# Kernel optimization log

Measured on AMD Instinct MI355X. Metric: run time of the kernel, lower is better.

The kernel has to match this reference:

```python
import jax, jax.numpy as jnp
import numpy as np

D_MODEL = 2048
N_HEADS = 16
HEAD_DIM = D_MODEL // N_HEADS  # 128
B, S = 4, 2048


def setup_inputs() -> dict:
    key = jax.random.key(0)
    ks = jax.random.split(key, 7)
    scale = 1.0 / np.sqrt(D_MODEL)
    return {
        "x": jax.random.normal(ks[0], (B, S, D_MODEL), dtype=jnp.float32),
        "cos": jax.random.uniform(ks[1], (S, HEAD_DIM // 2), dtype=jnp.float32),
        "sin": jax.random.uniform(ks[2], (S, HEAD_DIM // 2), dtype=jnp.float32),
        "Wq": jax.random.normal(ks[3], (D_MODEL, D_MODEL), dtype=jnp.float32) * scale,
        "Wk": jax.random.normal(ks[4], (D_MODEL, D_MODEL), dtype=jnp.float32) * scale,
        "Wv": jax.random.normal(ks[5], (D_MODEL, D_MODEL), dtype=jnp.float32) * scale,
        "Wo": jax.random.normal(ks[6], (D_MODEL, D_MODEL), dtype=jnp.float32) * scale,
    }


def apply_rope(x, cos, sin):
    # x: [B, H, S, head_dim]; cos/sin: [S, half] (split-in-half RoPE)
    half = x.shape[-1] // 2
    x1, x2 = x[..., :half], x[..., half:]
    cos = cos[None, None, :, :].astype(x.dtype)
    sin = sin[None, None, :, :].astype(x.dtype)
    return jnp.concatenate([x1 * cos - x2 * sin, x1 * sin + x2 * cos], axis=-1)


def reference(x, cos, sin, Wq, Wk, Wv, Wo):
    Bx, Sx, _ = x.shape
    # nn.Linear: y = x @ W.T
    def proj(W):
        y = jnp.einsum("bsd,ed->bse", x, W)
        return y.reshape(Bx, Sx, N_HEADS, HEAD_DIM).transpose(0, 2, 1, 3)  # [B,H,S,hd]
    q = apply_rope(proj(Wq), cos, sin)
    k = apply_rope(proj(Wk), cos, sin)
    v = proj(Wv)
    scale = 1.0 / np.sqrt(HEAD_DIM)
    scores = jnp.einsum("bhqd,bhkd->bhqk", q, k) * scale  # [B,H,S,S]
    attn = jax.nn.softmax(scores, axis=-1)
    out = jnp.einsum("bhqk,bhkd->bhqd", attn, v)
    out = out.transpose(0, 2, 1, 3).reshape(Bx, Sx, D_MODEL)
    return jnp.einsum("bsd,ed->bse", out, Wo)
```

## Files before the change

### kernel.cpp

```cpp
#include <hip/hip_runtime.h>

typedef _Float16 half_t;
typedef __attribute__((ext_vector_type(8))) _Float16 half8;
typedef __attribute__((ext_vector_type(4))) _Float16 half4v;
typedef __attribute__((ext_vector_type(4))) float f32x4;

#define MFMA16(a,b,c) __builtin_amdgcn_mfma_f32_16x16x32_f16((a),(b),(c),0,0,0)

__device__ __forceinline__ void gld_lds16(const half_t* g, half_t* l){
    __builtin_amdgcn_global_load_lds((__attribute__((address_space(1))) void*)(g),
                                     (__attribute__((address_space(3))) void*)(l), 16, 0, 0);
}

__global__ __launch_bounds__(256) void cvt_k(const float* __restrict__ s, half_t* __restrict__ d, int n4){
    int i = blockIdx.x * 256 + threadIdx.x;
    if (i < n4){
        float4 v = ((const float4*)s)[i];
        half4v h = { (half_t)v.x, (half_t)v.y, (half_t)v.z, (half_t)v.w };
        ((half4v*)d)[i] = h;
    }
}

__global__ __launch_bounds__(256) void cvtw_k(const float* __restrict__ w0, const float* __restrict__ w1,
                                              const float* __restrict__ w2, const float* __restrict__ w3,
                                              half_t* __restrict__ dst){
    const float* srcs[4] = {w0, w1, w2, w3};
    const float* s = srcs[blockIdx.y];
    int i = blockIdx.x * 256 + threadIdx.x;
    float4 v = ((const float4*)s)[i];
    half4v h = { (half_t)v.x, (half_t)v.y, (half_t)v.z, (half_t)v.w };
    ((half4v*)(dst))[(size_t)blockIdx.y * 1048576 + i] = h;
}

#define VMWAIT_(n) asm volatile("s_waitcnt vmcnt(" #n ")" ::: "memory")
#define VMWAIT(n)  VMWAIT_(n)

#define STAGE8(hh) { \
    const int Tt2 = (hh) >> 2, jj2 = (hh) & 3; \
    half_t* db = smem + ((jj2 & 1) << 15) + ((Tt2 & 1) << 14) + ((jj2 >> 1) << 13); \
    const half_t* Gs = ((jj2 & 1) ? Bg : Ag) + Tt2*64 + ((jj2 >> 1) << 5); \
    gld_lds16(Gs + off0, db + d0); \
    gld_lds16(Gs + off1, db + d1); \
}

#define PHASE8(Tt, jj, hh, VMN) { \
    half_t* Ah = smem + (((Tt) & 1) << 14) + (((jj) >> 1) << 13); \
    half_t* Bh = Ah + 32768; \
    half8 af[4], bf[4]; \
    _Pragma("unroll") for (int x = 0; x < 4; x++) af[x] = *(const half8*)(Ah + (((jj)&1)*4 + x)*1024 + cA); \
    _Pragma("unroll") for (int y = 0; y < 4; y++) bf[y] = *(const half8*)(Bh + y*1024 + cB); \
    if ((hh) < 128) STAGE8(hh); \
    if ((jj) & 1) VMWAIT(VMN); \
    asm volatile("s_barrier" ::: "memory"); \
    __builtin_amdgcn_s_setprio(1); \
    _Pragma("unroll") for (int x = 0; x < 4; x++) \
      _Pragma("unroll") for (int y = 0; y < 4; y++) \
        acc[((jj)&1)*4 + x][y] = MFMA16(af[x], bf[y], acc[((jj)&1)*4 + x][y]); \
    __builtin_amdgcn_s_setprio(0); \
    __builtin_amdgcn_sched_barrier(0); \
    asm volatile("s_barrier" ::: "memory"); \
}

__global__ __launch_bounds__(512) void gemm8(const half_t* __restrict__ A, const half_t* __restrict__ B,
                                             half_t* __restrict__ Qw, half_t* __restrict__ Kw,
                                             half_t* __restrict__ Vt, float* __restrict__ Co, int kind){
    const int tid  = threadIdx.x;
    const int lane = tid & 63;
    const int w4   = lane >> 4;
    const int l15  = lane & 15;
    const int l7   = lane & 7;
    const int wav  = tid >> 6;
    const int wavM = wav >> 2;
    const int wnq  = wav & 3;

    const int nwg = gridDim.x;
    const int wg  = blockIdx.x;
    const int swz = (wg & 7) * (nwg >> 3) + (wg >> 3);
    const int bm  = swz & 31;
    const int bn  = swz >> 5;

    __shared__ __align__(16) half_t smem[65536];

    const half_t* Ag = A + (size_t)bm * 256 * 2048;
    const half_t* Bg = B + (size_t)bn * 256 * 2048;

    const int p0  = tid >> 3, q0 = tid & 7, c0 = q0 ^ (p0 & 7);
    const int off0 = (p0 + ((c0 >> 2) << 7)) * 2048 + ((c0 & 3) << 3);
    const int off1 = off0 + 131072;
    const int d0  = tid * 8, d1 = d0 + 4096;

    const int cA = l15*64 + (((w4 | (wavM << 2)) ^ l7) << 3);
    const int cB = ((wnq & 1)*64 + l15)*64 + (((w4 | ((wnq >> 1) << 2)) ^ l7) << 3);

    f32x4 acc[8][4] = {};

#pragma unroll
    for (int h = 0; h < 6; h++) STAGE8(h);
    VMWAIT(4);
    asm volatile("s_barrier" ::: "memory");

    for (int it = 0; it < 15; it++){
        const int h0 = it*8 + 6;
        PHASE8(2*it,   0, h0,     6); PHASE8(2*it,   1, h0 + 1, 6);
        PHASE8(2*it,   2, h0 + 2, 6); PHASE8(2*it,   3, h0 + 3, 6);
        PHASE8(2*it+1, 0, h0 + 4, 6); PHASE8(2*it+1, 1, h0 + 5, 6);
        PHASE8(2*it+1, 2, h0 + 6, 6); PHASE8(2*it+1, 3, h0 + 7, 6);
    }
    PHASE8(30, 0, 126, 6); PHASE8(30, 1, 127, 6);
    PHASE8(30, 2, 128, 6); PHASE8(30, 3, 129, 2);
    PHASE8(31, 0, 130, 0); PHASE8(31, 1, 131, 0);
    PHASE8(31, 2, 132, 0); PHASE8(31, 3, 133, 0);

    const int mB = bm*256 + wavM*128 + w4*4;
    const int nB = bn*256 + wnq*64 + l15;

    if (kind == 0){
#pragma unroll
        for (int mi = 0; mi < 8; mi++)
#pragma unroll
            for (int ni = 0; ni < 4; ni++){
                int n  = nB + ni*16;
                int which = n >> 11;
                int nb = n & 2047;
                int m0 = mB + mi*16;
                if (which < 2){
                    half_t* dst = which ? Kw : Qw;
#pragma unroll
                    for (int r = 0; r < 4; r++){
                        int m = m0 + r;
                        dst[(((size_t)(m >> 11)*16 + (nb >> 7))*2048 + (m & 2047))*128 + (nb & 127)] = (half_t)acc[mi][ni][r];
                    }
                } else {
                    half4v hv = {(half_t)acc[mi][ni][0], (half_t)acc[mi][ni][1],
                                 (half_t)acc[mi][ni][2], (half_t)acc[mi][ni][3]};
                    *(half4v*)(Vt + (((size_t)(m0 >> 11)*16 + (nb >> 7))*128 + (nb & 127))*2048 + (m0 & 2047)) = hv;
                }
            }
    } else {
#pragma unroll
        for (int mi = 0; mi < 8; mi++)
#pragma unroll
            for (int ni = 0; ni < 4; ni++){
                int n  = nB + ni*16;
                int m0 = mB + mi*16;
#pragma unroll
                for (int r = 0; r < 4; r++)
                    Co[(size_t)(m0 + r)*2048 + n] = acc[mi][ni][r];
            }
    }
}

__global__ __launch_bounds__(256) void rope_k(half_t* __restrict__ Qw, half_t* __restrict__ Kw,
                                              const float* __restrict__ cs, const float* __restrict__ sn){
    int t  = blockIdx.x * 256 + threadIdx.x;
    int d  = t & 63;
    int s  = (t >> 6) & 2047;
    int bh = t >> 17;
    float c  = cs[s*64 + d];
    float si = sn[s*64 + d];
    size_t base = ((size_t)bh*2048 + s)*128 + d;
    float q1 = (float)Qw[base], q2 = (float)Qw[base+64];
    Qw[base]    = (half_t)(q1*c - q2*si);
    Qw[base+64] = (half_t)(q1*si + q2*c);
    float k1 = (float)Kw[base], k2 = (float)Kw[base+64];
    Kw[base]    = (half_t)(k1*c - k2*si);
    Kw[base+64] = (half_t)(k1*si + k2*c);
}

__global__ __launch_bounds__(256, 3) void attn_k(const half_t* __restrict__ Q, const half_t* __restrict__ K,
                                                 const half_t* __restrict__ Vt, half_t* __restrict__ AO){
    const int tid  = threadIdx.x;
    const int lane = tid & 63;
    const int w    = lane >> 4;
    const int l15  = lane & 15;
    const int l7   = lane & 7;
    const int wav  = tid >> 6;
    const int qt   = blockIdx.x;
    const int bh   = blockIdx.y;

    __shared__ __align__(16) half_t smem[8192 + 8192 + 4*2304];
    half_t* Ks = smem;
    half_t* Vs = smem + 8192;
    half_t* Ps = smem + 16384 + wav*2304;
    half_t* Ob = smem + wav*4096;

    const half_t* Qb = Q + ((size_t)bh*2048 + qt*128 + wav*32)*128;
    half8 aq[2][4];
#pragma unroll
    for (int qi = 0; qi < 2; qi++)
#pragma unroll
        for (int ks = 0; ks < 4; ks++)
            aq[qi][ks] = *(const half8*)(Qb + (qi*16 + l15)*128 + ks*32 + w*8);

    f32x4 oacc[8][2] = {};
    float m_[2] = {-1e30f, -1e30f};
    float l_[2] = {0.0f, 0.0f};

    const float SSC = 0.08838834764831845f * 1.4426950408889634f;

    for (int kt = 0; kt < 32; kt++){
        const half_t* Kb = K  + ((size_t)bh*2048 + kt*64)*128;
        const half_t* Vb = Vt + (size_t)bh*128*2048 + kt*64;
        __syncthreads();
#pragma unroll
        for (int i = 0; i < 4; i++){
            int c = tid + i*256;
            int key = c >> 4, pc = c & 15;
            gld_lds16(Kb + key*128 + ((pc ^ (key&7)) << 3), Ks + c*8);
        }
#pragma unroll
        for (int i = 0; i < 4; i++){
            int c = tid + i*256;
            int d = c >> 3, pc = c & 7;
            gld_lds16(Vb + (size_t)d*2048 + ((pc ^ (d&7)) << 3), Vs + c*8);
        }
        __syncthreads();

        f32x4 sacc[4][2] = {};
#pragma unroll
        for (int ks = 0; ks < 4; ks++){
#pragma unroll
            for (int t = 0; t < 4; t++){
                half8 kf = *(const half8*)(Ks + (t*16 + l15)*128 + (((ks*4 + w) ^ l7) << 3));
                sacc[t][0] = MFMA16(kf, aq[0][ks], sacc[t][0]);
                sacc[t][1] = MFMA16(kf, aq[1][ks], sacc[t][1]);
            }
        }

#pragma unroll
        for (int qi = 0; qi < 2; qi++){
            float mx = sacc[0][qi][0];
#pragma unroll
            for (int t = 0; t < 4; t++)
#pragma unroll
                for (int r = 0; r < 4; r++) mx = fmaxf(mx, sacc[t][qi][r]);
            mx = fmaxf(mx, __shfl_xor(mx, 16));
            mx = fmaxf(mx, __shfl_xor(mx, 32));
            float mxs = mx * SSC;
            unsigned long long upd = __ballot(mxs > m_[qi]);
            if (upd){
                float mn    = fmaxf(m_[qi], mxs);
                float alpha = exp2f(m_[qi] - mn);
                m_[qi] = mn;
                l_[qi] *= alpha;
#pragma unroll
                for (int t = 0; t < 8; t++)
#pragma unroll
                    for (int r = 0; r < 4; r++) oacc[t][qi][r] *= alpha;
            }
            float mq = m_[qi];
            float sum = 0.0f;
#pragma unroll
            for (int t = 0; t < 4; t++){
                float p0 = exp2f(sacc[t][qi][0]*SSC - mq);
                float p1 = exp2f(sacc[t][qi][1]*SSC - mq);
                float p2 = exp2f(sacc[t][qi][2]*SSC - mq);
                float p3 = exp2f(sacc[t][qi][3]*SSC - mq);
                sum += (p0 + p1) + (p2 + p3);
                half4v hv = {(half_t)p0, (half_t)p1, (half_t)p2, (half_t)p3};
                *(half4v*)(Ps + (qi*16 + l15)*72 + t*16 + w*4) = hv;
            }
            sum += __shfl_xor(sum, 16);
            sum += __shfl_xor(sum, 32);
            l_[qi] += sum;
        }

#pragma unroll
        for (int c2 = 0; c2 < 2; c2++){
            half8 pf0 = *(const half8*)(Ps + l15*72        + c2*32 + w*8);
            half8 pf1 = *(const half8*)(Ps + (16 + l15)*72 + c2*32 + w*8);
#pragma unroll
            for (int t = 0; t < 8; t++){
                half8 vf = *(const half8*)(Vs + (t*16 + l15)*64 + (((c2*4 + w) ^ l7) << 3));
                oacc[t][0] = MFMA16(vf, pf0, oacc[t][0]);
                oacc[t][1] = MFMA16(vf, pf1, oacc[t][1]);
            }
        }
    }

    float inv[2] = {1.0f / l_[0], 1.0f / l_[1]};
    __syncthreads();
#pragma unroll
    for (int t = 0; t < 8; t++)
#pragma unroll
        for (int qi = 0; qi < 2; qi++){
            int q  = qi*16 + l15;
            int c8 = t*2 + (w>>1);
            int pc = c8 ^ l7;
            half4v hv = {(half_t)(oacc[t][qi][0]*inv[qi]), (half_t)(oacc[t][qi][1]*inv[qi]),
                         (half_t)(oacc[t][qi][2]*inv[qi]), (half_t)(oacc[t][qi][3]*inv[qi])};
            *(half4v*)(Ob + q*128 + pc*8 + (w&1)*4) = hv;
        }
    const int b = bh >> 4, h = bh & 15;
#pragma unroll
    for (int it = 0; it < 8; it++){
        int q  = it*4 + w;
        half8 rd = *(const half8*)(Ob + q*128 + ((l15 ^ (q&7)) << 3));
        int s = qt*128 + wav*32 + q;
        *(half8*)(AO + ((size_t)(b*2048 + s))*2048 + h*128 + l15*8) = rd;
    }
}

extern "C" void kernel_launch(void* const* d_in, const int* in_sizes, int n_in,
                              void* d_out, int out_size, void* d_ws, size_t ws_size,
                              hipStream_t stream){
    const float* x  = (const float*)d_in[0];
    const float* cs = (const float*)d_in[1];
    const float* sn = (const float*)d_in[2];
    const float* Wq = (const float*)d_in[3];
    const float* Wk = (const float*)d_in[4];
    const float* Wv = (const float*)d_in[5];
    const float* Wo = (const float*)d_in[6];

    half_t* ws = (half_t*)d_ws;
    half_t* xh = ws;
    half_t* w4 = ws + (size_t)16777216;
    half_t* qw = ws + (size_t)33554432;
    half_t* kw = ws + (size_t)50331648;
    half_t* vt = ws + (size_t)67108864;
    half_t* ao = ws + (size_t)83886080;

    cvt_k<<<16384, 256, 0, stream>>>(x, xh, 4194304);
    cvtw_k<<<dim3(4096, 4), 256, 0, stream>>>(Wq, Wk, Wv, Wo, w4);

    gemm8<<<768, 512, 0, stream>>>(xh, w4, qw, kw, vt, nullptr, 0);
    rope_k<<<32768, 256, 0, stream>>>(qw, kw, cs, sn);
    attn_k<<<dim3(16, 64), 256, 0, stream>>>(qw, kw, vt, ao);
    gemm8<<<256, 512, 0, stream>>>(ao, w4 + 12582912, nullptr, nullptr, nullptr,
                                   (float*)d_out, 1);
}
```

Before: 733.4 us.

## Register-prefetch next K/V tile in attention, fold scale into Q, remap blocks

The attention kernel now loads the next K/V tile into registers while computing the current one, then writes it to LDS after a barrier. This replaces the synchronous direct-to-LDS loads that stalled every iteration. The softmax scale is pre-multiplied into Q in fp16, which removes per-element multiplies but adds a small rounding risk. The grid is flattened and remapped so that consecutive blocks spread across heads, with the aim of improving cache locality. The register staging costs extra VGPRs and may reduce occupancy.

```diff
diff --git a/kernel.cpp b/kernel.cpp
--- a/kernel.cpp
+++ b/kernel.cpp
@@ -175,8 +175,9 @@
     const int l15  = lane & 15;
     const int l7   = lane & 7;
     const int wav  = tid >> 6;
-    const int qt   = blockIdx.x;
-    const int bh   = blockIdx.y;
+    const int bid  = blockIdx.x;
+    const int qt   = (bid >> 3) & 15;
+    const int bh   = (bid & 7) * 8 + (bid >> 7);
 
     __shared__ __align__(16) half_t smem[8192 + 8192 + 4*2304];
     half_t* Ks = smem;
@@ -184,37 +185,57 @@
     half_t* Ps = smem + 16384 + wav*2304;
     half_t* Ob = smem + wav*4096;
 
+    const float SSC = 0.08838834764831845f * 1.4426950408889634f;
+
     const half_t* Qb = Q + ((size_t)bh*2048 + qt*128 + wav*32)*128;
     half8 aq[2][4];
 #pragma unroll
     for (int qi = 0; qi < 2; qi++)
 #pragma unroll
-        for (int ks = 0; ks < 4; ks++)
-            aq[qi][ks] = *(const half8*)(Qb + (qi*16 + l15)*128 + ks*32 + w*8);
+        for (int ks = 0; ks < 4; ks++){
+            half8 t = *(const half8*)(Qb + (qi*16 + l15)*128 + ks*32 + w*8);
+            aq[qi][ks] = t * (half_t)SSC;
+        }
+
+    int koff[4], voff[4], soff[4];
+#pragma unroll
+    for (int i = 0; i < 4; i++){
+        int c = tid + i*256;
+        int key = c >> 4, pk = c & 15;
+        koff[i] = key*128 + ((pk ^ (key & 7)) << 3);
+        int d = c >> 3, pv = c & 7;
+        voff[i] = (d << 11) + ((pv ^ (d & 7)) << 3);
+        soff[i] = c * 8;
+    }
+
+    const half_t* Kbase = K  + (size_t)bh*2048*128;
+    const half_t* Vbase = Vt + (size_t)bh*128*2048;
+
+    float4 kst[4], vst[4];
+#pragma unroll
+    for (int i = 0; i < 4; i++) kst[i] = *(const float4*)(Kbase + koff[i]);
+#pragma unroll
+    for (int i = 0; i < 4; i++) vst[i] = *(const float4*)(Vbase + voff[i]);
+#pragma unroll
+    for (int i = 0; i < 4; i++) *(float4*)(Ks + soff[i]) = kst[i];
+#pragma unroll
+    for (int i = 0; i < 4; i++) *(float4*)(Vs + soff[i]) = vst[i];
+    __syncthreads();
 
     f32x4 oacc[8][2] = {};
     float m_[2] = {-1e30f, -1e30f};
     float l_[2] = {0.0f, 0.0f};
 
-    const float SSC = 0.08838834764831845f * 1.4426950408889634f;
-
     for (int kt = 0; kt < 32; kt++){
-        const half_t* Kb = K  + ((size_t)bh*2048 + kt*64)*128;
-        const half_t* Vb = Vt + (size_t)bh*128*2048 + kt*64;
-        __syncthreads();
-#pragma unroll
-        for (int i = 0; i < 4; i++){
-            int c = tid + i*256;
-            int key = c >> 4, pc = c & 15;
-            gld_lds16(Kb + key*128 + ((pc ^ (key&7)) << 3), Ks + c*8);
-        }
-#pragma unroll
-        for (int i = 0; i < 4; i++){
-            int c = tid + i*256;
-            int d = c >> 3, pc = c & 7;
-            gld_lds16(Vb + (size_t)d*2048 + ((pc ^ (d&7)) << 3), Vs + c*8);
-        }
-        __syncthreads();
+        if (kt < 31){
+            const half_t* Kb = Kbase + (kt + 1)*64*128;
+            const half_t* Vb = Vbase + (kt + 1)*64;
+#pragma unroll
+            for (int i = 0; i < 4; i++) kst[i] = *(const float4*)(Kb + koff[i]);
+#pragma unroll
+            for (int i = 0; i < 4; i++) vst[i] = *(const float4*)(Vb + voff[i]);
+        }
+        __builtin_amdgcn_sched_barrier(0);
 
         f32x4 sacc[4][2] = {};
 #pragma unroll
@@ -236,10 +257,9 @@
                 for (int r = 0; r < 4; r++) mx = fmaxf(mx, sacc[t][qi][r]);
             mx = fmaxf(mx, __shfl_xor(mx, 16));
             mx = fmaxf(mx, __shfl_xor(mx, 32));
-            float mxs = mx * SSC;
-            unsigned long long upd = __ballot(mxs > m_[qi]);
+            unsigned long long upd = __ballot(mx > m_[qi]);
             if (upd){
-                float mn    = fmaxf(m_[qi], mxs);
+                float mn    = fmaxf(m_[qi], mx);
                 float alpha = exp2f(m_[qi] - mn);
                 m_[qi] = mn;
                 l_[qi] *= alpha;
@@ -252,10 +272,10 @@
             float sum = 0.0f;
 #pragma unroll
             for (int t = 0; t < 4; t++){
-                float p0 = exp2f(sacc[t][qi][0]*SSC - mq);
-                float p1 = exp2f(sacc[t][qi][1]*SSC - mq);
-                float p2 = exp2f(sacc[t][qi][2]*SSC - mq);
-                float p3 = exp2f(sacc[t][qi][3]*SSC - mq);
+                float p0 = exp2f(sacc[t][qi][0] - mq);
+                float p1 = exp2f(sacc[t][qi][1] - mq);
+                float p2 = exp2f(sacc[t][qi][2] - mq);
+                float p3 = exp2f(sacc[t][qi][3] - mq);
                 sum += (p0 + p1) + (p2 + p3);
                 half4v hv = {(half_t)p0, (half_t)p1, (half_t)p2, (half_t)p3};
                 *(half4v*)(Ps + (qi*16 + l15)*72 + t*16 + w*4) = hv;
@@ -276,10 +296,18 @@
                 oacc[t][1] = MFMA16(vf, pf1, oacc[t][1]);
             }
         }
+
+        __syncthreads();
+        if (kt < 31){
+#pragma unroll
+            for (int i = 0; i < 4; i++) *(float4*)(Ks + soff[i]) = kst[i];
+#pragma unroll
+            for (int i = 0; i < 4; i++) *(float4*)(Vs + soff[i]) = vst[i];
+        }
+        __syncthreads();
     }
 
     float inv[2] = {1.0f / l_[0], 1.0f / l_[1]};
-    __syncthreads();
 #pragma unroll
     for (int t = 0; t < 8; t++)
 #pragma unroll
@@ -325,7 +353,7 @@
 
     gemm8<<<768, 512, 0, stream>>>(xh, w4, qw, kw, vt, nullptr, 0);
     rope_k<<<32768, 256, 0, stream>>>(qw, kw, cs, sn);
-    attn_k<<<dim3(16, 64), 256, 0, stream>>>(qw, kw, vt, ao);
+    attn_k<<<1024, 256, 0, stream>>>(qw, kw, vt, ao);
     gemm8<<<256, 512, 0, stream>>>(ao, w4 + 12582912, nullptr, nullptr, nullptr,
                                    (float*)d_out, 1);
 }
```

After: 1.238 ms. +68.9%, slower.
